# Performance work log

Hardware: AMD Instinct MI355X
Metric: run time of the kernel (lower is better)

The kernel has to match this reference:

```python
import jax, jax.numpy as jnp
import numpy as np

NEG_INF = -jnp.inf


def setup_inputs() -> dict:
    B, T, E, H = 16, 1024, 1024, 1024  # batch, seq, embed_dim, head_dim (T <= H required by original buffer slicing)
    key = jax.random.key(0)
    k1, k2, k3, k4, k5, k6 = jax.random.split(key, 6)
    return {
        "key": jax.random.normal(k1, (B, T, E), dtype=jnp.float32),
        "query": jax.random.normal(k2, (B, T, E), dtype=jnp.float32),
        "value": jax.random.normal(k3, (B, T, E), dtype=jnp.float32),
        "padding_mask": jnp.zeros((B, 1, T), dtype=jnp.int32),
        # nn.Linear(embed_dim, head_dim, bias=False) weights: [head_dim, embed_dim]
        "Wk": jax.random.normal(k4, (H, E), dtype=jnp.float32) * (E ** -0.5),
        "Wq": jax.random.normal(k5, (H, E), dtype=jnp.float32) * (E ** -0.5),
        "Wv": jax.random.normal(k6, (H, E), dtype=jnp.float32) * (E ** -0.5),
    }


def reference(key, query, value, padding_mask, Wk, Wq, Wv):
    # key/query/value: [B, T, E]; W*: [H, E]
    B, T, E = key.shape
    k = jnp.einsum("bte,he->bth", key, Wk)
    q = jnp.einsum("bte,he->bth", query, Wq)
    v = jnp.einsum("bte,he->bth", value, Wv)
    # NOTE: original scales by d_k = key.size(-1) = embed_dim, not head_dim
    scale = 1.0 / jnp.sqrt(jnp.float32(E))
    qk = jnp.einsum("bth,bsh->bts", q, k) * scale  # [B, T, T]
    # causal buffer is tril(ones, diagonal=1): position i can attend to j <= i+1
    causal = jnp.tril(jnp.ones((T, T), dtype=jnp.float32), k=1)
    qk = jnp.where(causal == 0, NEG_INF, qk)
    qk = jnp.where(padding_mask == 1, NEG_INF, qk)  # padding_mask broadcasts [B,1,T] -> [B,T,T]
    p = jax.nn.softmax(qk, axis=-1)
    attn = jnp.einsum("bts,bsh->bth", p, v)  # dropout is identity in eval mode
    return attn
```

## Files before the change

### kernel.cpp

```cpp
#include <hip/hip_runtime.h>
#include <hip/hip_bf16.h>
#include <stdint.h>

typedef __bf16 bf16;
typedef __attribute__((ext_vector_type(8))) __bf16 bf16x8;
typedef __attribute__((ext_vector_type(4))) __bf16 bf16x4;
typedef __attribute__((ext_vector_type(4))) float  f32x4;

static __device__ __forceinline__ void gll16(const void* g, void* lds_base) {
  __builtin_amdgcn_global_load_lds((__attribute__((address_space(1))) void*)g,
                                   (__attribute__((address_space(3))) void*)lds_base,
                                   16, 0, 0);
}

#define MFMA_CLUSTER(MQ)                                                       \
  __builtin_amdgcn_s_barrier();                                                \
  asm volatile("s_waitcnt lgkmcnt(0)" ::: "memory");                           \
  __builtin_amdgcn_sched_barrier(0);                                           \
  __builtin_amdgcn_s_setprio(1);                                               \
  _Pragma("unroll") for (int i_ = 0; i_ < 4; ++i_)                             \
  _Pragma("unroll") for (int n_ = 0; n_ < 4; ++n_)                             \
  _Pragma("unroll") for (int kh_ = 0; kh_ < 2; ++kh_)                          \
    acc[(MQ) * 4 + i_][n_] = __builtin_amdgcn_mfma_f32_16x16x32_bf16(          \
        af[i_][kh_], bfr[n_][kh_], acc[(MQ) * 4 + i_][n_], 0, 0, 0);           \
  __builtin_amdgcn_s_setprio(0);

template <int VARIANT>
__global__ __launch_bounds__(512, 2) void gemm8(const bf16* __restrict__ A,
                                                const bf16* __restrict__ B,
                                                bf16* __restrict__ Cb,
                                                float* __restrict__ Cf,
                                                const int* __restrict__ pad) {
  extern __shared__ char smem[];
  char* ldsA = smem;
  char* ldsB = smem + 65536;

  const int tid = threadIdx.x;
  const int lane = tid & 63, wave = tid >> 6;
  const int lo = lane & 15, hi = lane >> 4;
  const int wmi = wave >> 2, wni = wave & 3;
  const int swz = (lo & 7) << 4;

  const int nwg = gridDim.x;
  const int id = (blockIdx.x % 8) * (nwg >> 3) + blockIdx.x / 8;

  int row0, col0, nt, b = 0;
  if (VARIANT <= 1) {
    row0 = (id >> 2) * 256; col0 = (id & 3) * 256; nt = 16;
  } else {
    b = id >> 4;
    const int r = id & 15, it = r >> 2, jt = r & 3;
    row0 = it * 256; col0 = jt * 256;
    nt = (VARIANT == 3) ? min(16, 6 + 4 * it) : 16;
    if (VARIANT == 2 && jt > it) {
      bf16* Sb = Cb + ((size_t)b << 20);
      const bf16 NI = (bf16)(-__builtin_inff());
      bf16x8 fill = { NI, NI, NI, NI, NI, NI, NI, NI };
#pragma unroll
      for (int q = 0; q < 16; ++q) {
        const int off = (q * 512 + tid) * 8;
        const int rr = off >> 8, cc = off & 255;
        *(bf16x8*)(Sb + (size_t)(row0 + rr) * 1024 + col0 + cc) = fill;
      }
      return;
    }
  }
  const bf16* Ap = A + ((size_t)b << 20) + (size_t)row0 * 1024;
  const bf16* Bp = B + ((size_t)b << 20) + (size_t)col0 * 1024;
  const int ntm1 = nt - 1;

  auto stgA = [&](int tidx, int slot) {
    const int tc = tidx > ntm1 ? ntm1 : tidx;
#pragma unroll
    for (int r = 0; r < 4; ++r) {
      const int x  = (wave * 4 + r) * 1024 + lane * 16;
      const int xs = x ^ (((x >> 7) & 7) << 4);
      gll16((const char*)Ap + (size_t)(xs >> 7) * 2048 + (size_t)tc * 128 + (xs & 127),
            ldsA + slot * 32768 + (wave * 4 + r) * 1024);
    }
  };
  auto stgB = [&](int tidx, int slot) {
    const int tc = tidx > ntm1 ? ntm1 : tidx;
#pragma unroll
    for (int r = 0; r < 4; ++r) {
      const int x  = (wave * 4 + r) * 1024 + lane * 16;
      const int xs = x ^ (((x >> 7) & 7) << 4);
      gll16((const char*)Bp + (size_t)(xs >> 7) * 2048 + (size_t)tc * 128 + (xs & 127),
            ldsB + slot * 32768 + (wave * 4 + r) * 1024);
    }
  };

  f32x4 acc[8][4] = {};

  stgB(0, 0);
  stgA(0, 0);
  stgB(1, 1);
  asm volatile("s_waitcnt vmcnt(4)" ::: "memory");
  __builtin_amdgcn_s_barrier();

  bf16x8 af[4][2], bfr[4][2];
#pragma unroll 2
  for (int u = 0; u < nt; ++u) {
    const int cur = u & 1;
#pragma unroll
    for (int i_ = 0; i_ < 4; ++i_)
#pragma unroll
      for (int kh_ = 0; kh_ < 2; ++kh_) {
        const int row_ = wmi * 128 + i_ * 16 + lo;
        af[i_][kh_] = *(const bf16x8*)(ldsA + cur * 32768 +
                                       ((row_ * 128 + kh_ * 64 + hi * 16) ^ swz));
      }
#pragma unroll
    for (int n_ = 0; n_ < 4; ++n_)
#pragma unroll
      for (int kh_ = 0; kh_ < 2; ++kh_) {
        const int row_ = wni * 64 + n_ * 16 + lo;
        bfr[n_][kh_] = *(const bf16x8*)(ldsB + cur * 32768 +
                                        ((row_ * 128 + kh_ * 64 + hi * 16) ^ swz));
      }
    stgA(u + 1, cur ^ 1);
    MFMA_CLUSTER(0)
    __builtin_amdgcn_s_barrier();
#pragma unroll
    for (int i_ = 0; i_ < 4; ++i_)
#pragma unroll
      for (int kh_ = 0; kh_ < 2; ++kh_) {
        const int row_ = wmi * 128 + 64 + i_ * 16 + lo;
        af[i_][kh_] = *(const bf16x8*)(ldsA + cur * 32768 +
                                       ((row_ * 128 + kh_ * 64 + hi * 16) ^ swz));
      }
    stgB(u + 2, cur);
    MFMA_CLUSTER(1)
    asm volatile("s_waitcnt vmcnt(4)" ::: "memory");
    __builtin_amdgcn_s_barrier();
  }

  if (VARIANT == 0) {
#pragma unroll
    for (int m = 0; m < 8; ++m)
#pragma unroll
      for (int n = 0; n < 4; ++n) {
        const int c = col0 + wni * 64 + n * 16 + lo;
        const int rbase = row0 + wmi * 128 + m * 16 + hi * 4;
#pragma unroll
        for (int j = 0; j < 4; ++j)
          Cb[(size_t)(rbase + j) * 1024 + c] = (bf16)acc[m][n][j];
      }
  } else if (VARIANT == 1) {
#pragma unroll
    for (int m = 0; m < 8; ++m)
#pragma unroll
      for (int n = 0; n < 4; ++n) {
        const int r = row0 + wmi * 128 + m * 16 + hi * 4;
        const int c = col0 + wni * 64 + n * 16 + lo;
        const int bb = r >> 10, tt = r & 1023;
        bf16x4 h = { (bf16)acc[m][n][0], (bf16)acc[m][n][1],
                     (bf16)acc[m][n][2], (bf16)acc[m][n][3] };
        *(bf16x4*)(Cb + ((size_t)bb << 20) + ((size_t)c << 10) + tt) = h;
      }
  } else if (VARIANT == 2) {
    const float NINF = -__builtin_inff();
#pragma unroll
    for (int n = 0; n < 4; ++n) {
      const int s = col0 + wni * 64 + n * 16 + lo;
      const int pd = pad[(b << 10) + s];
#pragma unroll
      for (int m = 0; m < 8; ++m) {
        const int tbase = row0 + wmi * 128 + m * 16 + hi * 4;
#pragma unroll
        for (int j = 0; j < 4; ++j) {
          float v = acc[m][n][j] * 0.03125f;
          if (s > tbase + j + 1 || pd != 0) v = NINF;
          Cb[((size_t)b << 20) + (size_t)(tbase + j) * 1024 + s] = (bf16)v;
        }
      }
    }
  } else {
#pragma unroll
    for (int m = 0; m < 8; ++m)
#pragma unroll
      for (int n = 0; n < 4; ++n) {
        const int h2 = col0 + wni * 64 + n * 16 + lo;
        const int tbase = row0 + wmi * 128 + m * 16 + hi * 4;
#pragma unroll
        for (int j = 0; j < 4; ++j)
          Cf[((size_t)b << 20) + (size_t)(tbase + j) * 1024 + h2] = acc[m][n][j];
      }
  }
  asm volatile("s_waitcnt vmcnt(0)" ::: "memory");
}

__global__ __launch_bounds__(256) void cvt_kernel(const float* __restrict__ src,
                                                  bf16* __restrict__ dst, int n) {
  const int i = (blockIdx.x * 256 + threadIdx.x) * 8;
  if (i >= n) return;
  const f32x4 a = *(const f32x4*)(src + i);
  const f32x4 b = *(const f32x4*)(src + i + 4);
  bf16x8 o = { (bf16)a[0], (bf16)a[1], (bf16)a[2], (bf16)a[3],
               (bf16)b[0], (bf16)b[1], (bf16)b[2], (bf16)b[3] };
  *(bf16x8*)(dst + i) = o;
}

__global__ __launch_bounds__(64) void corner_kernel(const bf16* __restrict__ Q,
                                                    const bf16* __restrict__ K,
                                                    const int* __restrict__ pad,
                                                    bf16* __restrict__ S) {
  const int b = blockIdx.x / 3, it = blockIdx.x % 3;
  const int t = it * 256 + 255, s = (it + 1) * 256;
  const int lane = threadIdx.x;
  const bf16* q = Q + ((size_t)b << 20) + (size_t)t * 1024 + lane * 16;
  const bf16* k = K + ((size_t)b << 20) + (size_t)s * 1024 + lane * 16;
  bf16x8 q0 = *(const bf16x8*)q, q1 = *(const bf16x8*)(q + 8);
  bf16x8 k0 = *(const bf16x8*)k, k1 = *(const bf16x8*)(k + 8);
  float d = 0.f;
#pragma unroll
  for (int j = 0; j < 8; ++j) d += (float)q0[j] * (float)k0[j] + (float)q1[j] * (float)k1[j];
#pragma unroll
  for (int o = 32; o; o >>= 1) d += __shfl_xor(d, o, 64);
  if (lane == 0) {
    float v = d * 0.03125f;
    if (pad[(b << 10) + s] != 0) v = -__builtin_inff();
    S[((size_t)b << 20) + (size_t)t * 1024 + s] = (bf16)v;
  }
}

__global__ __launch_bounds__(256) void softmax_kernel(bf16* __restrict__ S) {
  const int row  = blockIdx.x * 4 + (threadIdx.x >> 6);
  const int lane = threadIdx.x & 63;
  bf16* r = S + (size_t)row * 1024 + lane * 16;
  bf16x8 v0 = *(const bf16x8*)r;
  bf16x8 v1 = *(const bf16x8*)(r + 8);
  float f[16];
#pragma unroll
  for (int j = 0; j < 8; ++j) { f[j] = (float)v0[j]; f[8 + j] = (float)v1[j]; }
  float m = f[0];
#pragma unroll
  for (int j = 1; j < 16; ++j) m = fmaxf(m, f[j]);
#pragma unroll
  for (int o = 32; o; o >>= 1) m = fmaxf(m, __shfl_xor(m, o, 64));
  float sum = 0.f;
#pragma unroll
  for (int j = 0; j < 16; ++j) { f[j] = __expf(f[j] - m); sum += f[j]; }
#pragma unroll
  for (int o = 32; o; o >>= 1) sum += __shfl_xor(sum, o, 64);
  const float inv = 1.0f / sum;
#pragma unroll
  for (int j = 0; j < 8; ++j) { v0[j] = (bf16)(f[j] * inv); v1[j] = (bf16)(f[8 + j] * inv); }
  *(bf16x8*)r = v0;
  *(bf16x8*)(r + 8) = v1;
}

extern "C" void kernel_launch(void* const* d_in, const int* in_sizes, int n_in,
                              void* d_out, int out_size, void* d_ws, size_t ws_size,
                              hipStream_t stream) {
  const float* key   = (const float*)d_in[0];
  const float* query = (const float*)d_in[1];
  const float* value = (const float*)d_in[2];
  const int*   pad   = (const int*)d_in[3];
  const float* Wk    = (const float*)d_in[4];
  const float* Wq    = (const float*)d_in[5];
  const float* Wv    = (const float*)d_in[6];
  float* out = (float*)d_out;

  bf16* Wkb = (bf16*)d_ws;
  bf16* Wqb = Wkb + (1 << 20);
  bf16* Wvb = Wqb + (1 << 20);
  bf16* qb  = Wvb + (1 << 20);
  bf16* kb  = qb  + (16 << 20);
  bf16* vT  = kb  + (16 << 20);
  bf16* S   = vT  + (16 << 20);
  bf16* Xb  = S;

  hipFuncSetAttribute(reinterpret_cast<const void*>(&gemm8<0>),
                      hipFuncAttributeMaxDynamicSharedMemorySize, 131072);
  hipFuncSetAttribute(reinterpret_cast<const void*>(&gemm8<1>),
                      hipFuncAttributeMaxDynamicSharedMemorySize, 131072);
  hipFuncSetAttribute(reinterpret_cast<const void*>(&gemm8<2>),
                      hipFuncAttributeMaxDynamicSharedMemorySize, 131072);
  hipFuncSetAttribute(reinterpret_cast<const void*>(&gemm8<3>),
                      hipFuncAttributeMaxDynamicSharedMemorySize, 131072);

  cvt_kernel<<<512, 256, 0, stream>>>(Wk, Wkb, 1 << 20);
  cvt_kernel<<<512, 256, 0, stream>>>(Wq, Wqb, 1 << 20);
  cvt_kernel<<<512, 256, 0, stream>>>(Wv, Wvb, 1 << 20);

  cvt_kernel<<<8192, 256, 0, stream>>>(query, Xb, 16 << 20);
  gemm8<0><<<256, 512, 131072, stream>>>(Xb, Wqb, qb, nullptr, nullptr);
  cvt_kernel<<<8192, 256, 0, stream>>>(key, Xb, 16 << 20);
  gemm8<0><<<256, 512, 131072, stream>>>(Xb, Wkb, kb, nullptr, nullptr);
  cvt_kernel<<<8192, 256, 0, stream>>>(value, Xb, 16 << 20);
  gemm8<1><<<256, 512, 131072, stream>>>(Xb, Wvb, vT, nullptr, nullptr);

  gemm8<2><<<256, 512, 131072, stream>>>(qb, kb, S, nullptr, pad);
  corner_kernel<<<48, 64, 0, stream>>>(qb, kb, pad, S);
  softmax_kernel<<<4096, 256, 0, stream>>>(S);
  gemm8<3><<<256, 512, 131072, stream>>>(S, vT, nullptr, out, nullptr);
}
```

Before: 261.2 us.

## Fuse fp32-to-bf16 conversion into projection GEMMs and skip masked causal work

Projection GEMMs now read the fp32 inputs directly through registers, convert them to bf16 and write them to LDS, which removes three full-size conversion kernels and their intermediate buffer traffic. The K-loop is restructured into four MFMA quarter-blocks per k-tile with finer-grained staging. Tiles of S lying entirely above the causal band are no longer written, and the band-edge tile is filled with zeros instead of -inf. Softmax reads and writes only the valid causal prefix of each row. The register-staged A path adds VGPR pressure and more barriers per tile, and correctness now depends on the later GEMM never reading the unwritten S regions.

```diff
diff --git a/kernel.cpp b/kernel.cpp
--- a/kernel.cpp
+++ b/kernel.cpp
@@ -13,24 +13,18 @@
                                    16, 0, 0);
 }
 
-#define MFMA_CLUSTER(MQ)                                                       \
-  __builtin_amdgcn_s_barrier();                                                \
-  asm volatile("s_waitcnt lgkmcnt(0)" ::: "memory");                           \
-  __builtin_amdgcn_sched_barrier(0);                                           \
-  __builtin_amdgcn_s_setprio(1);                                               \
-  _Pragma("unroll") for (int i_ = 0; i_ < 4; ++i_)                             \
-  _Pragma("unroll") for (int n_ = 0; n_ < 4; ++n_)                             \
-  _Pragma("unroll") for (int kh_ = 0; kh_ < 2; ++kh_)                          \
-    acc[(MQ) * 4 + i_][n_] = __builtin_amdgcn_mfma_f32_16x16x32_bf16(          \
-        af[i_][kh_], bfr[n_][kh_], acc[(MQ) * 4 + i_][n_], 0, 0, 0);           \
-  __builtin_amdgcn_s_setprio(0);
+#define BARR  __builtin_amdgcn_s_barrier()
+#define VMW(N) asm volatile("s_waitcnt vmcnt(" #N ")" ::: "memory")
+#define LGKM0 do { asm volatile("s_waitcnt lgkmcnt(0)" ::: "memory");          \
+                   __builtin_amdgcn_sched_barrier(0); } while (0)
 
 template <int VARIANT>
-__global__ __launch_bounds__(512, 2) void gemm8(const bf16* __restrict__ A,
+__global__ __launch_bounds__(512, 2) void gemm8(const void* __restrict__ Araw,
                                                 const bf16* __restrict__ B,
                                                 bf16* __restrict__ Cb,
                                                 float* __restrict__ Cf,
                                                 const int* __restrict__ pad) {
+  constexpr bool FP32A = (VARIANT <= 1);
   extern __shared__ char smem[];
   char* ldsA = smem;
   char* ldsB = smem + 65536;
@@ -51,89 +45,136 @@
     b = id >> 4;
     const int r = id & 15, it = r >> 2, jt = r & 3;
     row0 = it * 256; col0 = jt * 256;
-    nt = (VARIANT == 3) ? min(16, 6 + 4 * it) : 16;
-    if (VARIANT == 2 && jt > it) {
+    nt = (VARIANT == 3) ? min(16, 4 * it + 6) : 16;
+    if (VARIANT == 2 && jt > it + 1) return;
+    if (VARIANT == 2 && jt == it + 1) {
       bf16* Sb = Cb + ((size_t)b << 20);
-      const bf16 NI = (bf16)(-__builtin_inff());
-      bf16x8 fill = { NI, NI, NI, NI, NI, NI, NI, NI };
+      bf16x8 z = {};
 #pragma unroll
       for (int q = 0; q < 16; ++q) {
         const int off = (q * 512 + tid) * 8;
-        const int rr = off >> 8, cc = off & 255;
-        *(bf16x8*)(Sb + (size_t)(row0 + rr) * 1024 + col0 + cc) = fill;
+        *(bf16x8*)(Sb + (size_t)(row0 + (off >> 8)) * 1024 + col0 + (off & 255)) = z;
       }
       return;
     }
   }
-  const bf16* Ap = A + ((size_t)b << 20) + (size_t)row0 * 1024;
-  const bf16* Bp = B + ((size_t)b << 20) + (size_t)col0 * 1024;
   const int ntm1 = nt - 1;
-
-  auto stgA = [&](int tidx, int slot) {
-    const int tc = tidx > ntm1 ? ntm1 : tidx;
-#pragma unroll
-    for (int r = 0; r < 4; ++r) {
-      const int x  = (wave * 4 + r) * 1024 + lane * 16;
+  const float* Afp = FP32A ? (const float*)Araw + (size_t)row0 * 1024 : nullptr;
+  const bf16*  Ab  = FP32A ? nullptr
+                           : (const bf16*)Araw + ((size_t)b << 20) + (size_t)row0 * 1024;
+  const bf16*  Bp  = B + (FP32A ? (size_t)0 : ((size_t)b << 20)) + (size_t)col0 * 1024;
+
+  f32x4 acc[8][4] = {};
+  bf16x8 af[4][2], b0[2][2], b1[2][2];
+  f32x4 rA0[4], rA1a[4], rA1b[4];
+
+  auto gllH = [&](const bf16* base, char* ldsOp, int h, int slot, int t) {
+    const int tc = t > ntm1 ? ntm1 : t;
+#pragma unroll
+    for (int r = 0; r < 2; ++r) {
+      const int x  = h * 16384 + (wave * 2 + r) * 1024 + lane * 16;
       const int xs = x ^ (((x >> 7) & 7) << 4);
-      gll16((const char*)Ap + (size_t)(xs >> 7) * 2048 + (size_t)tc * 128 + (xs & 127),
-            ldsA + slot * 32768 + (wave * 4 + r) * 1024);
+      gll16((const char*)base + (size_t)(xs >> 7) * 2048 + (size_t)tc * 128 + (xs & 127),
+            ldsOp + slot * 32768 + h * 16384 + (wave * 2 + r) * 1024);
     }
   };
-  auto stgB = [&](int tidx, int slot) {
-    const int tc = tidx > ntm1 ? ntm1 : tidx;
-#pragma unroll
-    for (int r = 0; r < 4; ++r) {
-      const int x  = (wave * 4 + r) * 1024 + lane * 16;
-      const int xs = x ^ (((x >> 7) & 7) << 4);
-      gll16((const char*)Bp + (size_t)(xs >> 7) * 2048 + (size_t)tc * 128 + (xs & 127),
-            ldsB + slot * 32768 + (wave * 4 + r) * 1024);
-    }
-  };
-
-  f32x4 acc[8][4] = {};
-
-  stgB(0, 0);
-  stgA(0, 0);
-  stgB(1, 1);
-  asm volatile("s_waitcnt vmcnt(4)" ::: "memory");
-  __builtin_amdgcn_s_barrier();
-
-  bf16x8 af[4][2], bfr[4][2];
-#pragma unroll 2
-  for (int u = 0; u < nt; ++u) {
-    const int cur = u & 1;
-#pragma unroll
-    for (int i_ = 0; i_ < 4; ++i_)
-#pragma unroll
-      for (int kh_ = 0; kh_ < 2; ++kh_) {
-        const int row_ = wmi * 128 + i_ * 16 + lo;
-        af[i_][kh_] = *(const bf16x8*)(ldsA + cur * 32768 +
-                                       ((row_ * 128 + kh_ * 64 + hi * 16) ^ swz));
-      }
-#pragma unroll
-    for (int n_ = 0; n_ < 4; ++n_)
-#pragma unroll
-      for (int kh_ = 0; kh_ < 2; ++kh_) {
-        const int row_ = wni * 64 + n_ * 16 + lo;
-        bfr[n_][kh_] = *(const bf16x8*)(ldsB + cur * 32768 +
-                                        ((row_ * 128 + kh_ * 64 + hi * 16) ^ swz));
-      }
-    stgA(u + 1, cur ^ 1);
-    MFMA_CLUSTER(0)
-    __builtin_amdgcn_s_barrier();
-#pragma unroll
-    for (int i_ = 0; i_ < 4; ++i_)
-#pragma unroll
-      for (int kh_ = 0; kh_ < 2; ++kh_) {
-        const int row_ = wmi * 128 + 64 + i_ * 16 + lo;
-        af[i_][kh_] = *(const bf16x8*)(ldsA + cur * 32768 +
-                                       ((row_ * 128 + kh_ * 64 + hi * 16) ^ swz));
-      }
-    stgB(u + 2, cur);
-    MFMA_CLUSTER(1)
-    asm volatile("s_waitcnt vmcnt(4)" ::: "memory");
-    __builtin_amdgcn_s_barrier();
-  }
+  auto glbA = [&](f32x4 rr[4], int h, int t) {
+    const int tc = t > ntm1 ? ntm1 : t;
+    const float* p = Afp + (size_t)(h * 128 + (tid >> 2)) * 1024 + (size_t)tc * 64 + (tid & 3) * 16;
+#pragma unroll
+    for (int j = 0; j < 4; ++j) rr[j] = *(const f32x4*)(p + j * 4);
+  };
+  auto wrA = [&](const f32x4 rr[4], int h, int slot) {
+    const int rowh = tid >> 2, colb = (tid & 3) * 32, key = (rowh & 7) << 4;
+    char* d = ldsA + slot * 32768 + h * 16384;
+    bf16x8 o0 = { (bf16)rr[0][0], (bf16)rr[0][1], (bf16)rr[0][2], (bf16)rr[0][3],
+                  (bf16)rr[1][0], (bf16)rr[1][1], (bf16)rr[1][2], (bf16)rr[1][3] };
+    bf16x8 o1 = { (bf16)rr[2][0], (bf16)rr[2][1], (bf16)rr[2][2], (bf16)rr[2][3],
+                  (bf16)rr[3][0], (bf16)rr[3][1], (bf16)rr[3][2], (bf16)rr[3][3] };
+    *(bf16x8*)(d + ((rowh * 128 + colb) ^ key)) = o0;
+    *(bf16x8*)(d + ((rowh * 128 + colb + 16) ^ key)) = o1;
+  };
+  auto rdA = [&](int mh, int slot) {
+#pragma unroll
+    for (int i = 0; i < 4; ++i)
+#pragma unroll
+      for (int kh = 0; kh < 2; ++kh) {
+        const int row = wmi * 128 + mh * 64 + i * 16 + lo;
+        af[i][kh] = *(const bf16x8*)(ldsA + slot * 32768 +
+                                     ((row * 128 + kh * 64 + hi * 16) ^ swz));
+      }
+  };
+  auto rdB = [&](bf16x8 dst[2][2], int nh, int slot) {
+#pragma unroll
+    for (int n = 0; n < 2; ++n)
+#pragma unroll
+      for (int kh = 0; kh < 2; ++kh) {
+        const int row = wni * 64 + nh * 32 + n * 16 + lo;
+        dst[n][kh] = *(const bf16x8*)(ldsB + slot * 32768 +
+                                      ((row * 128 + kh * 64 + hi * 16) ^ swz));
+      }
+  };
+  auto mmaQ = [&](bf16x8 bq[2][2], int mh, int nh) {
+    __builtin_amdgcn_s_setprio(1);
+#pragma unroll
+    for (int i = 0; i < 4; ++i)
+#pragma unroll
+      for (int n = 0; n < 2; ++n)
+#pragma unroll
+        for (int kh = 0; kh < 2; ++kh)
+          acc[mh * 4 + i][nh * 2 + n] = __builtin_amdgcn_mfma_f32_16x16x32_bf16(
+              af[i][kh], bq[n][kh], acc[mh * 4 + i][nh * 2 + n], 0, 0, 0);
+    __builtin_amdgcn_s_setprio(0);
+  };
+
+  if constexpr (FP32A) {
+    glbA(rA0, 0, 0);
+    glbA(rA1a, 1, 0);
+    glbA(rA1b, 0, 1);
+    VMW(8);  wrA(rA0, 0, 0);
+    VMW(4);  wrA(rA1a, 1, 0);
+    VMW(0);  wrA(rA1b, 0, 1);
+    gllH(Bp, ldsB, 0, 0, 0); gllH(Bp, ldsB, 1, 0, 0);
+    glbA(rA1b, 1, 1);
+    gllH(Bp, ldsB, 0, 1, 1); gllH(Bp, ldsB, 1, 1, 1);
+    VMW(8);
+    LGKM0; BARR;
+  } else {
+    gllH(Ab, ldsA, 0, 0, 0); gllH(Ab, ldsA, 1, 0, 0);
+    gllH(Bp, ldsB, 0, 0, 0); gllH(Bp, ldsB, 1, 0, 0);
+    gllH(Bp, ldsB, 0, 1, 1); gllH(Bp, ldsB, 1, 1, 1);
+    gllH(Ab, ldsA, 0, 1, 1);
+    VMW(6);
+    BARR;
+  }
+
+#define KTILE(U, CUR, RA1W, RA1L)                                              \
+                                                                       \
+  rdA(0, CUR); rdB(b0, 0, CUR);                                                \
+  if constexpr (FP32A) { glbA(rA0, 0, (U) + 2); }                              \
+  else { gllH(Ab, ldsA, 1, (CUR) ^ 1, (U) + 1); }                              \
+  BARR; LGKM0; mmaQ(b0, 0, 0); BARR;                                           \
+                                                                       \
+  rdB(b1, 1, CUR);                                                             \
+  if constexpr (FP32A) { VMW(8); wrA(RA1W, 1, (CUR) ^ 1); glbA(RA1L, 1, (U) + 2); } \
+  gllH(Bp, ldsB, 0, CUR, (U) + 2);                                             \
+  BARR; LGKM0; mmaQ(b1, 0, 1); BARR;                                           \
+                                                                       \
+  rdA(1, CUR);                                                                 \
+  gllH(Bp, ldsB, 1, CUR, (U) + 2);                                             \
+  BARR; LGKM0; mmaQ(b1, 1, 1); BARR;                                           \
+                                                                       \
+  if constexpr (FP32A) { VMW(8); wrA(rA0, 0, CUR); }                           \
+  else { gllH(Ab, ldsA, 0, CUR, (U) + 2); }                                    \
+  BARR; LGKM0; mmaQ(b0, 1, 0);                                                 \
+  if constexpr (!FP32A) { VMW(6); }                                            \
+  BARR;
+
+  for (int u = 0; u < nt; u += 2) {
+    KTILE(u,     0, rA1b, rA1a)
+    KTILE(u + 1, 1, rA1a, rA1b)
+  }
+#undef KTILE
 
   if (VARIANT == 0) {
 #pragma unroll
@@ -170,7 +211,8 @@
 #pragma unroll
         for (int j = 0; j < 4; ++j) {
           float v = acc[m][n][j] * 0.03125f;
-          if (s > tbase + j + 1 || pd != 0) v = NINF;
+          if (s > tbase + j + 1) v = 0.f;
+          else if (pd != 0) v = NINF;
           Cb[((size_t)b << 20) + (size_t)(tbase + j) * 1024 + s] = (bf16)v;
         }
       }
@@ -227,27 +269,42 @@
 __global__ __launch_bounds__(256) void softmax_kernel(bf16* __restrict__ S) {
   const int row  = blockIdx.x * 4 + (threadIdx.x >> 6);
   const int lane = threadIdx.x & 63;
+  const int t = row & 1023;
+  const int w = min(1024, t + 2);
+  const bool act = lane * 16 < w;
   bf16* r = S + (size_t)row * 1024 + lane * 16;
-  bf16x8 v0 = *(const bf16x8*)r;
-  bf16x8 v1 = *(const bf16x8*)(r + 8);
+  bf16x8 v0 = {}, v1 = {};
   float f[16];
 #pragma unroll
-  for (int j = 0; j < 8; ++j) { f[j] = (float)v0[j]; f[8 + j] = (float)v1[j]; }
+  for (int j = 0; j < 16; ++j) f[j] = -1e30f;
+  if (act) {
+    v0 = *(const bf16x8*)r;
+    v1 = *(const bf16x8*)(r + 8);
+#pragma unroll
+    for (int j = 0; j < 16; ++j)
+      if (lane * 16 + j < w) f[j] = (float)(j < 8 ? v0[j] : v1[j - 8]);
+  }
   float m = f[0];
 #pragma unroll
   for (int j = 1; j < 16; ++j) m = fmaxf(m, f[j]);
 #pragma unroll
   for (int o = 32; o; o >>= 1) m = fmaxf(m, __shfl_xor(m, o, 64));
   float sum = 0.f;
-#pragma unroll
-  for (int j = 0; j < 16; ++j) { f[j] = __expf(f[j] - m); sum += f[j]; }
+  float e[16];
+#pragma unroll
+  for (int j = 0; j < 16; ++j) { e[j] = __expf(f[j] - m); sum += e[j]; }
 #pragma unroll
   for (int o = 32; o; o >>= 1) sum += __shfl_xor(sum, o, 64);
   const float inv = 1.0f / sum;
-#pragma unroll
-  for (int j = 0; j < 8; ++j) { v0[j] = (bf16)(f[j] * inv); v1[j] = (bf16)(f[8 + j] * inv); }
-  *(bf16x8*)r = v0;
-  *(bf16x8*)(r + 8) = v1;
+  if (act) {
+#pragma unroll
+    for (int j = 0; j < 8; ++j) {
+      v0[j] = (bf16)(lane * 16 + j < w ? e[j] * inv : 0.f);
+      v1[j] = (bf16)(lane * 16 + 8 + j < w ? e[8 + j] * inv : 0.f);
+    }
+    *(bf16x8*)r = v0;
+    *(bf16x8*)(r + 8) = v1;
+  }
 }
 
 extern "C" void kernel_launch(void* const* d_in, const int* in_sizes, int n_in,
@@ -269,7 +326,6 @@
   bf16* kb  = qb  + (16 << 20);
   bf16* vT  = kb  + (16 << 20);
   bf16* S   = vT  + (16 << 20);
-  bf16* Xb  = S;
 
   hipFuncSetAttribute(reinterpret_cast<const void*>(&gemm8<0>),
                       hipFuncAttributeMaxDynamicSharedMemorySize, 131072);
@@ -284,15 +340,12 @@
   cvt_kernel<<<512, 256, 0, stream>>>(Wq, Wqb, 1 << 20);
   cvt_kernel<<<512, 256, 0, stream>>>(Wv, Wvb, 1 << 20);
 
-  cvt_kernel<<<8192, 256, 0, stream>>>(query, Xb, 16 << 20);
-  gemm8<0><<<256, 512, 131072, stream>>>(Xb, Wqb, qb, nullptr, nullptr);
-  cvt_kernel<<<8192, 256, 0, stream>>>(key, Xb, 16 << 20);
-  gemm8<0><<<256, 512, 131072, stream>>>(Xb, Wkb, kb, nullptr, nullptr);
-  cvt_kernel<<<8192, 256, 0, stream>>>(value, Xb, 16 << 20);
-  gemm8<1><<<256, 512, 131072, stream>>>(Xb, Wvb, vT, nullptr, nullptr);
-
-  gemm8<2><<<256, 512, 131072, stream>>>(qb, kb, S, nullptr, pad);
+  gemm8<0><<<256, 512, 131072, stream>>>((const void*)query, Wqb, qb, nullptr, nullptr);
+  gemm8<0><<<256, 512, 131072, stream>>>((const void*)key,   Wkb, kb, nullptr, nullptr);
+  gemm8<1><<<256, 512, 131072, stream>>>((const void*)value, Wvb, vT, nullptr, nullptr);
+
+  gemm8<2><<<256, 512, 131072, stream>>>((const void*)qb, kb, S, nullptr, pad);
   corner_kernel<<<48, 64, 0, stream>>>(qb, kb, pad, S);
   softmax_kernel<<<4096, 256, 0, stream>>>(S);
-  gemm8<3><<<256, 512, 131072, stream>>>(S, vT, nullptr, out, nullptr);
-}
+  gemm8<3><<<256, 512, 131072, stream>>>((const void*)S, vT, nullptr, out, nullptr);
+}
```

Result: slower. 352.8 us (+35.1%).
